# Optimization experiments

Hardware: AMD Instinct MI355X
Metric: run time of the kernel (lower is better)

## Reference

```python
import jax, jax.numpy as jnp
import numpy as np

BN_EPS = 1e-5
EPS = 1e-12
ALPHA = 0.1
ITERS = 3

def _bn(x, gamma, beta, axes):
    # BatchNorm with batch stats (track_running_stats=False), biased variance
    mean = x.mean(axis=axes, keepdims=True)
    var = x.var(axis=axes, keepdims=True)
    return (x - mean) * jax.lax.rsqrt(var + BN_EPS) * gamma + beta

def setup_inputs() -> dict:
    key = jax.random.key(0)
    ks = jax.random.split(key, 4)
    b, c, h, w = 64, 512, 64, 64
    n = 32  # embed_num
    x = jax.random.normal(ks[0], (b, c, h, w), dtype=jnp.float32)
    meta_embed = jax.random.normal(ks[1], (n, c), dtype=jnp.float32)
    Wq = jax.random.normal(ks[2], (c, c), dtype=jnp.float32) * (1.0 / np.sqrt(c))
    bq = jax.random.normal(ks[3], (c,), dtype=jnp.float32) * 0.01
    return {
        "x": x, "meta_embed": meta_embed, "Wq": Wq, "bq": bq,
        "g1": jnp.ones((c,), jnp.float32), "b1": jnp.zeros((c,), jnp.float32),
        "g2": jnp.ones((n,), jnp.float32), "b2": jnp.zeros((n,), jnp.float32),
    }

def reference(x, meta_embed, Wq, bq, g1, b1, g2, b2):
    b, c, h, w = x.shape
    d = c
    inputs = x.reshape(b, c, h * w).transpose(0, 2, 1)  # (b, hw, d)
    k = inputs
    v = inputs
    n = meta_embed.shape[0]
    slots = jnp.broadcast_to(meta_embed[None], (b, n, d))
    new_slots = None
    for _ in range(ITERS):
        if new_slots is not None:
            slots = new_slots * ALPHA + slots * (1.0 - ALPHA)
        # to_q: Linear -> BatchNorm1d over flattened (b*n, d) -> ReLU
        q = slots.reshape(b * n, d) @ Wq.T + bq
        q = jax.nn.relu(_bn(q, g1, b1, axes=0)).reshape(b, n, d)
        attn = jnp.einsum('bid,bjd->bij', q, k)  # (b, n, hw)
        # mask_norm: BatchNorm1d over channels=n (reduce batch & hw) -> ReLU
        attn = jax.nn.relu(_bn(attn, g2[None, :, None], b2[None, :, None], axes=(0, 2)))
        new_slots = jnp.einsum('bjd,bij->bid', v, attn) / (attn.sum(-1, keepdims=True) + EPS)
    return new_slots
```

## Files before the change

kernel.cpp:

```cpp
#include <hip/hip_runtime.h>


#define F4(p)  (*reinterpret_cast<float4*>(p))
#define CF4(p) (*reinterpret_cast<const float4*>(p))

#define O_SUM1 0
#define O_SQ1  512
#define O_SUM2 1024
#define O_SQ2  1056
#define O_SC1  1088
#define O_SH1  1600
#define O_SC2  2112
#define O_SH2  2144
#define O_RS   2176

typedef __attribute__((address_space(1))) const void gvoid_t;
typedef __attribute__((address_space(3))) void lvoid_t;
__device__ __forceinline__ void gload_lds16(const float* g, float* l) {
    __builtin_amdgcn_global_load_lds((gvoid_t*)g, (lvoid_t*)l, 16, 0, 0);
}

__global__ void k_init_slots(const float* __restrict__ meta, float* __restrict__ slots) {
    int f = blockIdx.x * 256 + threadIdx.x;
    int m = f >> 7;
    int d4 = f & 127;
    F4(slots + (size_t)f * 4) = CF4(meta + ((size_t)((m & 31) << 7) + d4) * 4);
}

__global__ void k_blend(float* __restrict__ slots, const float* __restrict__ ns) {
    int f = blockIdx.x * 256 + threadIdx.x;
    float4 s = F4(slots + (size_t)f * 4);
    float4 n = CF4(ns + (size_t)f * 4);
    s.x = 0.9f * s.x + 0.1f * n.x;
    s.y = 0.9f * s.y + 0.1f * n.y;
    s.z = 0.9f * s.z + 0.1f * n.z;
    s.w = 0.9f * s.w + 0.1f * n.w;
    F4(slots + (size_t)f * 4) = s;
}

__global__ void k_qinit(const float* __restrict__ bq, float* __restrict__ Q) {
    int f = blockIdx.x * 256 + threadIdx.x;
    F4(Q + (size_t)f * 4) = CF4(bq + (size_t)(f & 127) * 4);
}

__global__ void k_zero_out(float* __restrict__ out) {
    int f = blockIdx.x * 256 + threadIdx.x;
    float4 z = {0.f, 0.f, 0.f, 0.f};
    F4(out + (size_t)f * 4) = z;
}

__global__ __launch_bounds__(256) void k_qgemm(const float* __restrict__ S,
                                               const float* __restrict__ Wq,
                                               float* __restrict__ Q) {
    __shared__ __align__(16) float asT[32][36];
    __shared__ __align__(16) float bsT[32][516];
    const int m0 = blockIdx.x * 32;
    const int kbase = blockIdx.y * 128;
    const int t = threadIdx.x;
    const int ty = t >> 6, tx = t & 63;
    float c[8][8] = {};
    for (int ch = 0; ch < 4; ++ch) {
        int k0 = kbase + ch * 32;
        {
            int m = t >> 3, kq = t & 7;
            float4 v = CF4(S + (size_t)(m0 + m) * 512 + k0 + kq * 4);
            asT[kq * 4 + 0][m] = v.x; asT[kq * 4 + 1][m] = v.y;
            asT[kq * 4 + 2][m] = v.z; asT[kq * 4 + 3][m] = v.w;
        }
#pragma unroll
        for (int cc = 0; cc < 16; ++cc) {
            int lin = t + 256 * cc;
            int n = lin >> 3, kq = lin & 7;
            float4 v = CF4(Wq + (size_t)n * 512 + k0 + kq * 4);
            bsT[kq * 4 + 0][n] = v.x; bsT[kq * 4 + 1][n] = v.y;
            bsT[kq * 4 + 2][n] = v.z; bsT[kq * 4 + 3][n] = v.w;
        }
        __syncthreads();
#pragma unroll 8
        for (int k = 0; k < 32; ++k) {
            float4 a0 = F4(&asT[k][ty * 8]);
            float4 a1 = F4(&asT[k][ty * 8 + 4]);
            float4 b0 = F4(&bsT[k][tx * 4]);
            float4 b1 = F4(&bsT[k][256 + tx * 4]);
            float av[8] = {a0.x, a0.y, a0.z, a0.w, a1.x, a1.y, a1.z, a1.w};
            float bv[8] = {b0.x, b0.y, b0.z, b0.w, b1.x, b1.y, b1.z, b1.w};
#pragma unroll
            for (int ii = 0; ii < 8; ++ii)
#pragma unroll
                for (int jj = 0; jj < 8; ++jj)
                    c[ii][jj] = fmaf(av[ii], bv[jj], c[ii][jj]);
        }
        __syncthreads();
    }
#pragma unroll
    for (int ii = 0; ii < 8; ++ii) {
        float* dst = Q + (size_t)(m0 + ty * 8 + ii) * 512;
#pragma unroll
        for (int q = 0; q < 4; ++q) atomicAdd(dst + tx * 4 + q, c[ii][q]);
#pragma unroll
        for (int q = 0; q < 4; ++q) atomicAdd(dst + 256 + tx * 4 + q, c[ii][4 + q]);
    }
}

__global__ void k_zero_stats(float* __restrict__ stats) {
    int i = blockIdx.x * 256 + threadIdx.x;
    if (i < 1088) stats[i] = 0.0f;
}

__global__ __launch_bounds__(256) void k_bn1_stats(const float* __restrict__ Q,
                                                   float* __restrict__ stats) {
    int cg = blockIdx.x & 7, rc = blockIdx.x >> 3;
    int lc = threadIdx.x & 63;
    int col = cg * 64 + lc;
    int rsub = threadIdx.x >> 6;
    float s = 0.f, sq = 0.f;
    for (int k = 0; k < 64; ++k) {
        float v = Q[(size_t)(rc * 256 + rsub + 4 * k) * 512 + col];
        s += v;
        sq += v * v;
    }
    __shared__ float ls[4][64], lq[4][64];
    ls[rsub][lc] = s;
    lq[rsub][lc] = sq;
    __syncthreads();
    if (threadIdx.x < 64) {
        int tcol = threadIdx.x;
        float ts = ls[0][tcol] + ls[1][tcol] + ls[2][tcol] + ls[3][tcol];
        float tq = lq[0][tcol] + lq[1][tcol] + lq[2][tcol] + lq[3][tcol];
        atomicAdd(&stats[O_SUM1 + cg * 64 + tcol], ts);
        atomicAdd(&stats[O_SQ1 + cg * 64 + tcol], tq);
    }
}

__global__ void k_bn1_fin(float* __restrict__ stats, const float* __restrict__ g1,
                          const float* __restrict__ b1) {
    int c = threadIdx.x;
    float mean = stats[O_SUM1 + c] * (1.0f / 2048.0f);
    float var = stats[O_SQ1 + c] * (1.0f / 2048.0f) - mean * mean;
    float sc = rsqrtf(var + 1e-5f) * g1[c];
    stats[O_SC1 + c] = sc;
    stats[O_SH1 + c] = b1[c] - mean * sc;
}

__global__ void k_bn1_apply(float* __restrict__ Q, const float* __restrict__ stats) {
    int f = blockIdx.x * 256 + threadIdx.x;
    int col4 = f & 127;
    float4 v = F4(Q + (size_t)f * 4);
    float4 sc = CF4(stats + O_SC1 + col4 * 4);
    float4 sh = CF4(stats + O_SH1 + col4 * 4);
    v.x = fmaxf(fmaf(v.x, sc.x, sh.x), 0.f);
    v.y = fmaxf(fmaf(v.y, sc.y, sh.y), 0.f);
    v.z = fmaxf(fmaf(v.z, sc.z, sh.z), 0.f);
    v.w = fmaxf(fmaf(v.w, sc.w, sh.w), 0.f);
    F4(Q + (size_t)f * 4) = v;
}

__global__ __launch_bounds__(256) void k_gemm1(const float* __restrict__ Q,
                                               const float* __restrict__ X,
                                               float* __restrict__ attn) {
    __shared__ __align__(16) float qsT[32][36];
    __shared__ __align__(16) float xs[32][512];
    const int b = blockIdx.y;
    const int j0 = blockIdx.x * 512;
    const int t = threadIdx.x;
    const int w = t >> 6, l = t & 63;
    const int ty = w, tx = l;
    const float* qb = Q + (size_t)b * 32 * 512;
    const float* xb = X + (size_t)b * 512 * 4096 + j0;
    float c[8][8] = {};
    for (int k0 = 0; k0 < 512; k0 += 32) {
        {
            int i = t >> 3, kq = t & 7;
            float4 v = CF4(qb + (size_t)i * 512 + k0 + kq * 4);
            qsT[kq * 4 + 0][i] = v.x; qsT[kq * 4 + 1][i] = v.y;
            qsT[kq * 4 + 2][i] = v.z; qsT[kq * 4 + 3][i] = v.w;
        }
#pragma unroll
        for (int cc = 0; cc < 16; ++cc) {
            int chunk = w * 16 + cc;
            int row = chunk >> 1, half = chunk & 1;
            const float* src = xb + (size_t)(k0 + row) * 4096 + half * 256 + l * 4;
            gload_lds16(src, &xs[row][half * 256]);
        }
        __syncthreads();
#pragma unroll 8
        for (int k = 0; k < 32; ++k) {
            float4 a0 = F4(&qsT[k][ty * 8]);
            float4 a1 = F4(&qsT[k][ty * 8 + 4]);
            float4 b0 = F4(&xs[k][tx * 4]);
            float4 b1 = F4(&xs[k][256 + tx * 4]);
            float av[8] = {a0.x, a0.y, a0.z, a0.w, a1.x, a1.y, a1.z, a1.w};
            float bv[8] = {b0.x, b0.y, b0.z, b0.w, b1.x, b1.y, b1.z, b1.w};
#pragma unroll
            for (int ii = 0; ii < 8; ++ii)
#pragma unroll
                for (int jj = 0; jj < 8; ++jj)
                    c[ii][jj] = fmaf(av[ii], bv[jj], c[ii][jj]);
        }
        __syncthreads();
    }
#pragma unroll
    for (int ii = 0; ii < 8; ++ii) {
        float* dst = attn + (size_t)(b * 32 + ty * 8 + ii) * 4096 + j0;
        float4 r0 = {c[ii][0], c[ii][1], c[ii][2], c[ii][3]};
        float4 r1 = {c[ii][4], c[ii][5], c[ii][6], c[ii][7]};
        F4(dst + tx * 4) = r0;
        F4(dst + 256 + tx * 4) = r1;
    }
}

__global__ __launch_bounds__(256) void k_bn2_stats(const float* __restrict__ attn,
                                                   float* __restrict__ stats) {
    int i = blockIdx.x, b = blockIdx.y;
    const float* p = attn + (size_t)(b * 32 + i) * 4096;
    int t = threadIdx.x;
    float s = 0.f, sq = 0.f;
#pragma unroll
    for (int c = 0; c < 4; ++c) {
        float4 v = CF4(p + (size_t)(t + 256 * c) * 4);
        s += v.x + v.y + v.z + v.w;
        sq += v.x * v.x + v.y * v.y + v.z * v.z + v.w * v.w;
    }
    __shared__ float rs[256], rq[256];
    rs[t] = s; rq[t] = sq;
    __syncthreads();
    for (int off = 128; off > 0; off >>= 1) {
        if (t < off) { rs[t] += rs[t + off]; rq[t] += rq[t + off]; }
        __syncthreads();
    }
    if (t == 0) {
        atomicAdd(&stats[O_SUM2 + i], rs[0]);
        atomicAdd(&stats[O_SQ2 + i], rq[0]);
    }
}

__global__ void k_bn2_fin(float* __restrict__ stats, const float* __restrict__ g2,
                          const float* __restrict__ b2) {
    int i = threadIdx.x;
    const float inv = 1.0f / 262144.0f;
    float mean = stats[O_SUM2 + i] * inv;
    float var = stats[O_SQ2 + i] * inv - mean * mean;
    float sc = rsqrtf(var + 1e-5f) * g2[i];
    stats[O_SC2 + i] = sc;
    stats[O_SH2 + i] = b2[i] - mean * sc;
}

__global__ __launch_bounds__(256) void k_bn2_apply(float* __restrict__ attn,
                                                   float* __restrict__ stats) {
    int i = blockIdx.x, b = blockIdx.y;
    float* p = attn + (size_t)(b * 32 + i) * 4096;
    float sc = stats[O_SC2 + i], sh = stats[O_SH2 + i];
    int t = threadIdx.x;
    float s = 0.f;
#pragma unroll
    for (int c = 0; c < 4; ++c) {
        float4 v = F4(p + (size_t)(t + 256 * c) * 4);
        v.x = fmaxf(fmaf(v.x, sc, sh), 0.f);
        v.y = fmaxf(fmaf(v.y, sc, sh), 0.f);
        v.z = fmaxf(fmaf(v.z, sc, sh), 0.f);
        v.w = fmaxf(fmaf(v.w, sc, sh), 0.f);
        s += v.x + v.y + v.z + v.w;
        F4(p + (size_t)(t + 256 * c) * 4) = v;
    }
    __shared__ float rs[256];
    rs[t] = s;
    __syncthreads();
    for (int off = 128; off > 0; off >>= 1) {
        if (t < off) rs[t] += rs[t + off];
        __syncthreads();
    }
    if (t == 0) stats[O_RS + b * 32 + i] = rs[0];
}

__global__ __launch_bounds__(256) void k_gemm2(const float* __restrict__ attn,
                                               const float* __restrict__ X,
                                               const float* __restrict__ stats,
                                               float* __restrict__ out) {
    __shared__ __align__(16) float asT[32][36];
    __shared__ __align__(16) float xsT[32][516];
    const int b = blockIdx.y;
    const int jbase0 = blockIdx.x * 512;
    const int t = threadIdx.x;
    const int ty = t >> 6, tx = t & 63;
    const float* ab = attn + (size_t)b * 32 * 4096 + jbase0;
    const float* xb = X + (size_t)b * 512 * 4096 + jbase0;
    float c[8][8] = {};
    for (int ch = 0; ch < 16; ++ch) {
        int jb = ch * 32;
        {
            int i = t >> 3, jq = t & 7;
            float4 v = CF4(ab + (size_t)i * 4096 + jb + jq * 4);
            asT[jq * 4 + 0][i] = v.x; asT[jq * 4 + 1][i] = v.y;
            asT[jq * 4 + 2][i] = v.z; asT[jq * 4 + 3][i] = v.w;
        }
#pragma unroll
        for (int cc = 0; cc < 16; ++cc) {
            int lin = t + 256 * cc;
            int d = lin >> 3, jq = lin & 7;
            float4 v = CF4(xb + (size_t)d * 4096 + jb + jq * 4);
            xsT[jq * 4 + 0][d] = v.x; xsT[jq * 4 + 1][d] = v.y;
            xsT[jq * 4 + 2][d] = v.z; xsT[jq * 4 + 3][d] = v.w;
        }
        __syncthreads();
#pragma unroll 8
        for (int k = 0; k < 32; ++k) {
            float4 a0 = F4(&asT[k][ty * 8]);
            float4 a1 = F4(&asT[k][ty * 8 + 4]);
            float4 b0 = F4(&xsT[k][tx * 4]);
            float4 b1 = F4(&xsT[k][256 + tx * 4]);
            float av[8] = {a0.x, a0.y, a0.z, a0.w, a1.x, a1.y, a1.z, a1.w};
            float bv[8] = {b0.x, b0.y, b0.z, b0.w, b1.x, b1.y, b1.z, b1.w};
#pragma unroll
            for (int ii = 0; ii < 8; ++ii)
#pragma unroll
                for (int jj = 0; jj < 8; ++jj)
                    c[ii][jj] = fmaf(av[ii], bv[jj], c[ii][jj]);
        }
        __syncthreads();
    }
#pragma unroll
    for (int ii = 0; ii < 8; ++ii) {
        int row = b * 32 + ty * 8 + ii;
        float inv = 1.0f / (stats[O_RS + row] + 1e-12f);
        float* dst = out + (size_t)row * 512;
#pragma unroll
        for (int q = 0; q < 4; ++q) atomicAdd(dst + tx * 4 + q, c[ii][q] * inv);
#pragma unroll
        for (int q = 0; q < 4; ++q) atomicAdd(dst + 256 + tx * 4 + q, c[ii][4 + q] * inv);
    }
}

extern "C" void kernel_launch(void* const* d_in, const int* in_sizes, int n_in,
                              void* d_out, int out_size, void* d_ws, size_t ws_size,
                              hipStream_t stream) {
    const float* x    = (const float*)d_in[0];
    const float* meta = (const float*)d_in[1];
    const float* Wq   = (const float*)d_in[2];
    const float* bq   = (const float*)d_in[3];
    const float* g1   = (const float*)d_in[4];
    const float* b1   = (const float*)d_in[5];
    const float* g2   = (const float*)d_in[6];
    const float* b2   = (const float*)d_in[7];
    float* out = (float*)d_out;

    float* ws = (float*)d_ws;
    float* slots = ws;
    float* q     = ws + 1048576;
    float* attn  = ws + 2097152;
    float* stats = ws + 10485760;

    k_init_slots<<<1024, 256, 0, stream>>>(meta, slots);
    for (int it = 0; it < 3; ++it) {
        if (it > 0) k_blend<<<1024, 256, 0, stream>>>(slots, out);
        k_qinit<<<1024, 256, 0, stream>>>(bq, q);
        k_qgemm<<<dim3(64, 4), 256, 0, stream>>>(slots, Wq, q);
        k_zero_stats<<<5, 256, 0, stream>>>(stats);
        k_bn1_stats<<<64, 256, 0, stream>>>(q, stats);
        k_bn1_fin<<<1, 512, 0, stream>>>(stats, g1, b1);
        k_bn1_apply<<<1024, 256, 0, stream>>>(q, stats);
        k_gemm1<<<dim3(8, 64), 256, 0, stream>>>(q, x, attn);
        k_bn2_stats<<<dim3(32, 64), 256, 0, stream>>>(attn, stats);
        k_bn2_fin<<<1, 32, 0, stream>>>(stats, g2, b2);
        k_bn2_apply<<<dim3(32, 64), 256, 0, stream>>>(attn, stats);
        k_zero_out<<<1024, 256, 0, stream>>>(out);
        k_gemm2<<<dim3(8, 64), 256, 0, stream>>>(attn, x, stats, out);
    }
}
```

Measured before the change: 2.171 ms.

## Pre-transpose Wq and x once and stream tiles into LDS directly

After: 2.306 ms. 6.2% more time.

```diff
diff --git a/kernel.cpp b/kernel.cpp
--- a/kernel.cpp
+++ b/kernel.cpp
@@ -20,6 +20,37 @@
     __builtin_amdgcn_global_load_lds((gvoid_t*)g, (lvoid_t*)l, 16, 0, 0);
 }
 
+__global__ __launch_bounds__(256) void k_transpose64(const float* __restrict__ A,
+                                                     float* __restrict__ AT,
+                                                     int R, int C) {
+    __shared__ __align__(16) float tile[64][68];
+    const int cb = blockIdx.x * 64;
+    const int rb = blockIdx.y * 64;
+    const size_t bofs = (size_t)blockIdx.z * R * C;
+    const float* Ab = A + bofs;
+    float* ATb = AT + bofs;
+    const int t = threadIdx.x;
+    const int g = t >> 4, h = t & 15;
+    float4 v0 = CF4(Ab + (size_t)(rb + g * 4 + 0) * C + cb + h * 4);
+    float4 v1 = CF4(Ab + (size_t)(rb + g * 4 + 1) * C + cb + h * 4);
+    float4 v2 = CF4(Ab + (size_t)(rb + g * 4 + 2) * C + cb + h * 4);
+    float4 v3 = CF4(Ab + (size_t)(rb + g * 4 + 3) * C + cb + h * 4);
+    float4 w0 = {v0.x, v1.x, v2.x, v3.x};
+    float4 w1 = {v0.y, v1.y, v2.y, v3.y};
+    float4 w2 = {v0.z, v1.z, v2.z, v3.z};
+    float4 w3 = {v0.w, v1.w, v2.w, v3.w};
+    F4(&tile[h * 4 + 0][g * 4]) = w0;
+    F4(&tile[h * 4 + 1][g * 4]) = w1;
+    F4(&tile[h * 4 + 2][g * 4]) = w2;
+    F4(&tile[h * 4 + 3][g * 4]) = w3;
+    __syncthreads();
+#pragma unroll
+    for (int s = 0; s < 4; ++s) {
+        int crow = g + 16 * s;
+        F4(ATb + (size_t)(cb + crow) * R + rb + h * 4) = F4(&tile[crow][h * 4]);
+    }
+}
+
 __global__ void k_init_slots(const float* __restrict__ meta, float* __restrict__ slots) {
     int f = blockIdx.x * 256 + threadIdx.x;
     int m = f >> 7;
@@ -50,14 +81,15 @@
 }
 
 __global__ __launch_bounds__(256) void k_qgemm(const float* __restrict__ S,
-                                               const float* __restrict__ Wq,
+                                               const float* __restrict__ WqT,
                                                float* __restrict__ Q) {
     __shared__ __align__(16) float asT[32][36];
-    __shared__ __align__(16) float bsT[32][516];
+    __shared__ __align__(16) float bs[32][512];
     const int m0 = blockIdx.x * 32;
     const int kbase = blockIdx.y * 128;
     const int t = threadIdx.x;
-    const int ty = t >> 6, tx = t & 63;
+    const int w = t >> 6, l = t & 63;
+    const int ty = w, tx = l;
     float c[8][8] = {};
     for (int ch = 0; ch < 4; ++ch) {
         int k0 = kbase + ch * 32;
@@ -69,19 +101,18 @@
         }
 #pragma unroll
         for (int cc = 0; cc < 16; ++cc) {
-            int lin = t + 256 * cc;
-            int n = lin >> 3, kq = lin & 7;
-            float4 v = CF4(Wq + (size_t)n * 512 + k0 + kq * 4);
-            bsT[kq * 4 + 0][n] = v.x; bsT[kq * 4 + 1][n] = v.y;
-            bsT[kq * 4 + 2][n] = v.z; bsT[kq * 4 + 3][n] = v.w;
+            int chunk = w * 16 + cc;
+            int row = chunk >> 1, half = chunk & 1;
+            const float* src = WqT + (size_t)(k0 + row) * 512 + half * 256 + l * 4;
+            gload_lds16(src, &bs[row][half * 256]);
         }
         __syncthreads();
 #pragma unroll 8
         for (int k = 0; k < 32; ++k) {
             float4 a0 = F4(&asT[k][ty * 8]);
             float4 a1 = F4(&asT[k][ty * 8 + 4]);
-            float4 b0 = F4(&bsT[k][tx * 4]);
-            float4 b1 = F4(&bsT[k][256 + tx * 4]);
+            float4 b0 = F4(&bs[k][tx * 4]);
+            float4 b1 = F4(&bs[k][256 + tx * 4]);
             float av[8] = {a0.x, a0.y, a0.z, a0.w, a1.x, a1.y, a1.z, a1.w};
             float bv[8] = {b0.x, b0.y, b0.z, b0.w, b1.x, b1.y, b1.z, b1.w};
 #pragma unroll
@@ -273,17 +304,18 @@
 }
 
 __global__ __launch_bounds__(256) void k_gemm2(const float* __restrict__ attn,
-                                               const float* __restrict__ X,
+                                               const float* __restrict__ XT,
                                                const float* __restrict__ stats,
                                                float* __restrict__ out) {
     __shared__ __align__(16) float asT[32][36];
-    __shared__ __align__(16) float xsT[32][516];
+    __shared__ __align__(16) float xs[32][512];
     const int b = blockIdx.y;
     const int jbase0 = blockIdx.x * 512;
     const int t = threadIdx.x;
-    const int ty = t >> 6, tx = t & 63;
+    const int w = t >> 6, l = t & 63;
+    const int ty = w, tx = l;
     const float* ab = attn + (size_t)b * 32 * 4096 + jbase0;
-    const float* xb = X + (size_t)b * 512 * 4096 + jbase0;
+    const float* xb = XT + (size_t)b * 4096 * 512 + (size_t)jbase0 * 512;
     float c[8][8] = {};
     for (int ch = 0; ch < 16; ++ch) {
         int jb = ch * 32;
@@ -295,19 +327,18 @@
         }
 #pragma unroll
         for (int cc = 0; cc < 16; ++cc) {
-            int lin = t + 256 * cc;
-            int d = lin >> 3, jq = lin & 7;
-            float4 v = CF4(xb + (size_t)d * 4096 + jb + jq * 4);
-            xsT[jq * 4 + 0][d] = v.x; xsT[jq * 4 + 1][d] = v.y;
-            xsT[jq * 4 + 2][d] = v.z; xsT[jq * 4 + 3][d] = v.w;
+            int chunk = w * 16 + cc;
+            int row = chunk >> 1, half = chunk & 1;
+            const float* src = xb + (size_t)(jb + row) * 512 + half * 256 + l * 4;
+            gload_lds16(src, &xs[row][half * 256]);
         }
         __syncthreads();
 #pragma unroll 8
         for (int k = 0; k < 32; ++k) {
             float4 a0 = F4(&asT[k][ty * 8]);
             float4 a1 = F4(&asT[k][ty * 8 + 4]);
-            float4 b0 = F4(&xsT[k][tx * 4]);
-            float4 b1 = F4(&xsT[k][256 + tx * 4]);
+            float4 b0 = F4(&xs[k][tx * 4]);
+            float4 b1 = F4(&xs[k][256 + tx * 4]);
             float av[8] = {a0.x, a0.y, a0.z, a0.w, a1.x, a1.y, a1.z, a1.w};
             float bv[8] = {b0.x, b0.y, b0.z, b0.w, b1.x, b1.y, b1.z, b1.w};
 #pragma unroll
@@ -348,12 +379,17 @@
     float* q     = ws + 1048576;
     float* attn  = ws + 2097152;
     float* stats = ws + 10485760;
+    float* wqT   = ws + 10489984;
+    float* xT    = ws + 16777216;
+
+    k_transpose64<<<dim3(8, 8, 1), 256, 0, stream>>>(Wq, wqT, 512, 512);
+    k_transpose64<<<dim3(64, 8, 64), 256, 0, stream>>>(x, xT, 512, 4096);
 
     k_init_slots<<<1024, 256, 0, stream>>>(meta, slots);
     for (int it = 0; it < 3; ++it) {
         if (it > 0) k_blend<<<1024, 256, 0, stream>>>(slots, out);
         k_qinit<<<1024, 256, 0, stream>>>(bq, q);
-        k_qgemm<<<dim3(64, 4), 256, 0, stream>>>(slots, Wq, q);
+        k_qgemm<<<dim3(64, 4), 256, 0, stream>>>(slots, wqT, q);
         k_zero_stats<<<5, 256, 0, stream>>>(stats);
         k_bn1_stats<<<64, 256, 0, stream>>>(q, stats);
         k_bn1_fin<<<1, 512, 0, stream>>>(stats, g1, b1);
@@ -363,6 +399,6 @@
         k_bn2_fin<<<1, 32, 0, stream>>>(stats, g2, b2);
         k_bn2_apply<<<dim3(32, 64), 256, 0, stream>>>(attn, stats);
         k_zero_out<<<1024, 256, 0, stream>>>(out);
-        k_gemm2<<<dim3(8, 64), 256, 0, stream>>>(attn, x, stats, out);
-    }
-}
+        k_gemm2<<<dim3(8, 64), 256, 0, stream>>>(attn, xT, stats, out);
+    }
+}
```
